# Performance work log

Hardware: AMD Instinct MI355X
Metric: run time of the kernel (lower is better)

The kernel has to match this reference:

```python
import jax, jax.numpy as jnp
import numpy as np
from jax import lax

K = 3
PAD = 1
K2 = K * K


def _conv(x, w, b):
    dn = lax.conv_dimension_numbers(x.shape, w.shape, ('NCHW', 'OIHW', 'NCHW'))
    y = lax.conv_general_dilated(x, w, (1, 1), [(PAD, PAD), (PAD, PAD)], dimension_numbers=dn)
    return y + b[None, :, None, None]


def _gather(x, iy, ix):
    # x: [B,C,H,W]; iy,ix: [B,K2,H,W] int32 -> [B,C,K2,H,W]
    B, C, H, W = x.shape
    flat = x.reshape(B, C, H * W)
    idx = iy * W + ix  # [B,K2,H,W]
    return jax.vmap(lambda xb, ib: xb[:, ib])(flat, idx)


def _deform_conv2d(x, offset_w, offset_b, mask_w, mask_b, weight):
    B, C, H, W = x.shape
    O = weight.shape[0]
    offset = _conv(x, offset_w, offset_b)            # [B,2*K2,H,W]
    mask = jax.nn.sigmoid(_conv(x, mask_w, mask_b))  # [B,K2,H,W]

    off = offset.reshape(B, K2, 2, H, W)
    oy, ox = off[:, :, 0], off[:, :, 1]              # [B,K2,H,W]

    ki = (jnp.arange(K2) // K).astype(x.dtype)       # kernel row per tap
    kj = (jnp.arange(K2) % K).astype(x.dtype)        # kernel col per tap
    base_y = (jnp.arange(H) - PAD).astype(x.dtype)
    base_x = (jnp.arange(W) - PAD).astype(x.dtype)

    py = oy + base_y[None, None, :, None] + ki[None, :, None, None]  # [B,K2,H,W]
    px = ox + base_x[None, None, None, :] + kj[None, :, None, None]

    y0 = jnp.floor(py)
    x0 = jnp.floor(px)
    dy = py - y0
    dx = px - x0
    y0i = y0.astype(jnp.int32)
    x0i = x0.astype(jnp.int32)

    acc = jnp.zeros((B, C, K2, H, W), dtype=x.dtype)
    for (yc, xc, wgt) in [
        (y0i,     x0i,     (1 - dy) * (1 - dx)),
        (y0i,     x0i + 1, (1 - dy) * dx),
        (y0i + 1, x0i,     dy * (1 - dx)),
        (y0i + 1, x0i + 1, dy * dx),
    ]:
        valid = ((yc >= 0) & (yc < H) & (xc >= 0) & (xc < W)).astype(x.dtype)
        g = _gather(x, jnp.clip(yc, 0, H - 1), jnp.clip(xc, 0, W - 1))  # [B,C,K2,H,W]
        acc = acc + g * (wgt * valid)[:, None]

    modulated = acc * mask[:, None]                  # [B,C,K2,H,W]
    w2 = weight.reshape(O, C, K2)
    return jnp.einsum('bckhw,ock->bohw', modulated, w2)


def setup_inputs() -> dict:
    key = jax.random.key(0)
    ks = jax.random.split(key, 6)
    B, C, O, H, W = 4, 64, 64, 128, 128
    return {
        'x': jax.random.normal(ks[0], (B, C, H, W), jnp.float32),
        'offset_w': jax.random.normal(ks[1], (2 * K2, C, K, K), jnp.float32) * 0.05,
        'offset_b': jax.random.normal(ks[2], (2 * K2,), jnp.float32) * 0.05,
        'mask_w': jax.random.normal(ks[3], (K2, C, K, K), jnp.float32) * 0.05,
        'mask_b': jnp.full((K2,), 0.5, jnp.float32),
        'weight': jax.random.normal(ks[5], (O, C, K, K), jnp.float32) * (1.0 / np.sqrt(C * K2)),
    }


def reference(x, offset_w, offset_b, mask_w, mask_b, weight):
    return _deform_conv2d(x, offset_w, offset_b, mask_w, mask_b, weight)
```

## Files before the change

kernel.cpp:

```cpp
#include <hip/hip_runtime.h>
#include <math.h>

#define BB 4
#define CC 64
#define OO 64
#define HH 128
#define WW 128
#define HWsz (HH * WW)

typedef __attribute__((ext_vector_type(8))) _Float16 half8;
typedef __attribute__((ext_vector_type(4))) float floatx4;

__global__ __launch_bounds__(256) void pre_kernel(
    const float* __restrict__ x, const float* __restrict__ wgt,
    const float* __restrict__ ow, const float* __restrict__ mw,
    _Float16* __restrict__ xh, _Float16* __restrict__ waf,
    _Float16* __restrict__ wcf)
{
    int bid = blockIdx.x;
    int tid = threadIdx.x;
    if (bid < 512) {
        int b = bid >> 7, y = bid & 127;
        int px = tid & 127;
        int ch = (tid >> 7) * 32;
        const float* xp = x + (size_t)(b * CC + ch) * HWsz + y * WW + px;
        _Float16 buf[32];
#pragma unroll
        for (int q = 0; q < 32; ++q)
            buf[q] = (_Float16)xp[(size_t)q * HWsz];
        _Float16* dst = xh + ((size_t)(b * HH + y) * WW + px) * 64 + ch;
#pragma unroll
        for (int q = 0; q < 4; ++q)
            *(half8*)&dst[q * 8] = *(const half8*)&buf[q * 8];
    } else {
        int i = (bid - 512) * 256 + tid;
        if (i < 36864) {
            int j = i & 7, lane = (i >> 3) & 63, rest = i >> 9;
            int m = rest & 3, kh = (rest >> 2) & 1, k = rest >> 3;
            int o = m * 16 + (lane & 15);
            int c = kh * 32 + ((lane >> 4) << 3) + j;
            waf[i] = (_Float16)wgt[o * 576 + c * 9 + k];
        } else if (i < 55296) {
            int t = i - 36864;
            int j = t & 7, lane = (t >> 3) & 63, rest = t >> 9;
            int m = rest & 1, kh = (rest >> 1) & 1, k = rest >> 2;
            int o = m * 16 + (lane & 15);
            int c = kh * 32 + ((lane >> 4) << 3) + j;
            float v = 0.f;
            if (o < 18) v = ow[o * 576 + c * 9 + k];
            else if (o < 27) v = mw[(o - 18) * 576 + c * 9 + k];
            wcf[t] = (_Float16)v;
        }
    }
}

__global__ __launch_bounds__(1024, 1) void fused_kernel(
    const _Float16* __restrict__ xh, const _Float16* __restrict__ waf,
    const _Float16* __restrict__ wcf, const float* __restrict__ ob,
    const float* __restrict__ mb, float* __restrict__ out)
{
    __shared__ __align__(16) _Float16 lds_waf[36864];
    __shared__ _Float16 omh[16 * 27 * 16];
    __shared__ __align__(16) _Float16 blendb[16 * 2048];

    int tid = threadIdx.x;
    int gid = blockIdx.x;
    int sid = (gid & 7) * 32 + (gid >> 3);
    int b = sid >> 6;
    int t = sid & 63;
    int rq = t >> 1;
    int q = t & 1;

    int wv = tid >> 6;
    int lane = tid & 63;
    int s = wv & 3;
    int h = rq * 4 + (wv >> 2);
    int p0 = q << 6;
    int g = lane >> 4;
    int pl = lane & 15;
    int goff = g * 8;
    int xw = p0 + s * 16 + pl;
    int oct = lane & 7;
    int pxg = lane >> 3;

    const _Float16* xhb = xh + ((size_t)b << 20);
    _Float16* omw = &omh[wv * 27 * 16];
    _Float16* bbw = &blendb[wv * 2048];

    half8 stg[9];
    if (wv < 8) {
#pragma unroll
        for (int i = 0; i < 9; ++i)
            stg[i] = *(const half8*)(waf + ((wv * 9 + i) << 9) + lane * 8);
    }

    floatx4 accC0 = {0.f, 0.f, 0.f, 0.f};
    floatx4 accC1 = {0.f, 0.f, 0.f, 0.f};

#define CADDR(K, P, V) do {                                                  \
    int ky = (K) / 3, kx = (K) - ky * 3;                                     \
    int yy = h + ky - 1, xx = xw + kx - 1;                                   \
    V = (yy >= 0) & (yy < HH) & (xx >= 0) & (xx < WW);                       \
    int yc = min(max(yy, 0), HH - 1), xc = min(max(xx, 0), WW - 1);          \
    P = ((yc * WW + xc) << 6) + goff;                                        \
} while (0)

#define CONVTAP(K, S0, S1, V) do {                                           \
    const _Float16* wp = wcf + ((K) << 11) + lane * 8;                       \
    half8 w00 = *(const half8*)(wp + (0 << 9));                              \
    half8 w01 = *(const half8*)(wp + (1 << 9));                              \
    half8 w10 = *(const half8*)(wp + (2 << 9));                              \
    half8 w11 = *(const half8*)(wp + (3 << 9));                              \
    half8 z = {0, 0, 0, 0, 0, 0, 0, 0};                                     \
    half8 a0 = (V) ? S0 : z;                                                 \
    half8 a1 = (V) ? S1 : z;                                                 \
    accC0 = __builtin_amdgcn_mfma_f32_16x16x32_f16(w00, a0, accC0, 0, 0, 0); \
    accC1 = __builtin_amdgcn_mfma_f32_16x16x32_f16(w01, a0, accC1, 0, 0, 0); \
    accC0 = __builtin_amdgcn_mfma_f32_16x16x32_f16(w10, a1, accC0, 0, 0, 0); \
    accC1 = __builtin_amdgcn_mfma_f32_16x16x32_f16(w11, a1, accC1, 0, 0, 0); \
} while (0)

    {
        bool vA, vB;
        int pa, pb;
        half8 A0, A1, B0, B1;
        CADDR(0, pa, vA);
        A0 = *(const half8*)(xhb + pa);
        A1 = *(const half8*)(xhb + pa + 32);
#pragma unroll 1
        for (int kp = 0; kp < 4; ++kp) {
            int k = kp * 2;
            CADDR(k + 1, pb, vB);
            B0 = *(const half8*)(xhb + pb);
            B1 = *(const half8*)(xhb + pb + 32);
            CONVTAP(k, A0, A1, vA);
            CADDR(k + 2, pa, vA);
            A0 = *(const half8*)(xhb + pa);
            A1 = *(const half8*)(xhb + pa + 32);
            CONVTAP(k + 1, B0, B1, vB);
        }
        CONVTAP(8, A0, A1, vA);
    }

#pragma unroll
    for (int j = 0; j < 4; ++j) {
        int o = g * 4 + j;
        omw[o * 16 + pl] = (_Float16)(accC0[j] + ob[o]);
        int o2 = 16 + g * 4 + j;
        float v = accC1[j];
        if (o2 < 18) omw[o2 * 16 + pl] = (_Float16)(v + ob[o2]);
        else if (o2 < 27)
            omw[o2 * 16 + pl] =
                (_Float16)(1.0f / (1.0f + expf(-(v + mb[o2 - 18]))));
    }

    if (wv < 8) {
#pragma unroll
        for (int i = 0; i < 9; ++i)
            *(half8*)&lds_waf[((wv * 9 + i) << 9) + lane * 8] = stg[i];
    }
    __syncthreads();

    floatx4 acc0 = {0.f, 0.f, 0.f, 0.f}, acc1 = {0.f, 0.f, 0.f, 0.f};
    floatx4 acc2 = {0.f, 0.f, 0.f, 0.f}, acc3 = {0.f, 0.f, 0.f, 0.f};

#define MKT(K, P, U00, U01, U10, U11, I00, I01, I10, I11) do {               \
    int ky = (K) / 3, kx = (K) - ky * 3;                                     \
    float oy = (float)omw[(2 * (K)) * 16 + (P)];                             \
    float ox = (float)omw[(2 * (K) + 1) * 16 + (P)];                         \
    float mk = (float)omw[(18 + (K)) * 16 + (P)];                            \
    float py = oy + (float)(h + ky - 1);                                     \
    float qx = ox + (float)(p0 + s * 16 + (P) + kx - 1);                     \
    float y0f = floorf(py), x0f = floorf(qx);                                \
    float dyy = py - y0f, dxx = qx - x0f;                                    \
    int y0 = (int)y0f, x0 = (int)x0f;                                        \
    int y1 = y0 + 1, x1 = x0 + 1;                                            \
    bool vy0 = (y0 >= 0) & (y0 < HH), vy1 = (y1 >= 0) & (y1 < HH);           \
    bool vx0 = (x0 >= 0) & (x0 < WW), vx1 = (x1 >= 0) & (x1 < WW);           \
    U00 = (vy0 & vx0) ? (1.f - dyy) * (1.f - dxx) * mk : 0.f;                \
    U01 = (vy0 & vx1) ? (1.f - dyy) * dxx * mk : 0.f;                        \
    U10 = (vy1 & vx0) ? dyy * (1.f - dxx) * mk : 0.f;                        \
    U11 = (vy1 & vx1) ? dyy * dxx * mk : 0.f;                                \
    int yc0 = min(max(y0, 0), HH - 1), yc1 = min(max(y1, 0), HH - 1);        \
    int xc0 = min(max(x0, 0), WW - 1), xc1 = min(max(x1, 0), WW - 1);        \
    I00 = ((yc0 * WW + xc0) << 6) + oct * 8;                                 \
    I01 = ((yc0 * WW + xc1) << 6) + oct * 8;                                 \
    I10 = ((yc1 * WW + xc0) << 6) + oct * 8;                                 \
    I11 = ((yc1 * WW + xc1) << 6) + oct * 8;                                 \
} while (0)

#define SPLAT8(H) ((half8){(H), (H), (H), (H), (H), (H), (H), (H)})
#define MF(Q, B, A) A = __builtin_amdgcn_mfma_f32_16x16x32_f16(Q, B, A, 0, 0, 0)

#define TAP(K) do {                                                          \
    float uA0, uA1, uA2, uA3, uB0, uB1, uB2, uB3;                            \
    int iA0, iA1, iA2, iA3, iB0, iB1, iB2, iB3;                              \
    MKT(K, pxg, uA0, uA1, uA2, uA3, iA0, iA1, iA2, iA3);                     \
    MKT(K, 8 + pxg, uB0, uB1, uB2, uB3, iB0, iB1, iB2, iB3);                 \
    half8 a0 = *(const half8*)(xhb + iA0);                                   \
    half8 a1 = *(const half8*)(xhb + iA1);                                   \
    half8 a2 = *(const half8*)(xhb + iA2);                                   \
    half8 a3 = *(const half8*)(xhb + iA3);                                   \
    half8 e0 = *(const half8*)(xhb + iB0);                                   \
    half8 e1 = *(const half8*)(xhb + iB1);                                   \
    half8 e2 = *(const half8*)(xhb + iB2);                                   \
    half8 e3 = *(const half8*)(xhb + iB3);                                   \
    half8 bfA = a0 * SPLAT8((_Float16)uA0);                                  \
    bfA = bfA + a1 * SPLAT8((_Float16)uA1);                                  \
    bfA = bfA + a2 * SPLAT8((_Float16)uA2);                                  \
    bfA = bfA + a3 * SPLAT8((_Float16)uA3);                                  \
    half8 bfB = e0 * SPLAT8((_Float16)uB0);                                  \
    bfB = bfB + e1 * SPLAT8((_Float16)uB1);                                  \
    bfB = bfB + e2 * SPLAT8((_Float16)uB2);                                  \
    bfB = bfB + e3 * SPLAT8((_Float16)uB3);                                  \
    _Float16* bb = bbw + (((K) & 1) << 10);                                  \
    *(half8*)&bb[(pxg << 6) + ((oct ^ pxg) << 3)] = bfA;                     \
    *(half8*)&bb[((8 + pxg) << 6) + ((oct ^ pxg) << 3)] = bfB;               \
    half8 bf = *(const half8*)&bb[(pl << 6) + ((g ^ (pl & 7)) << 3)];        \
    half8 bd = *(const half8*)&bb[(pl << 6) + (((g + 4) ^ (pl & 7)) << 3)];  \
    const _Float16* wk = &lds_waf[((K) << 12) + lane * 8];                   \
    half8 q0 = *(const half8*)(wk + (0 << 9));                               \
    half8 q1 = *(const half8*)(wk + (1 << 9));                               \
    half8 q2 = *(const half8*)(wk + (2 << 9));                               \
    half8 q3 = *(const half8*)(wk + (3 << 9));                               \
    half8 q4 = *(const half8*)(wk + (4 << 9));                               \
    half8 q5 = *(const half8*)(wk + (5 << 9));                               \
    half8 q6 = *(const half8*)(wk + (6 << 9));                               \
    half8 q7 = *(const half8*)(wk + (7 << 9));                               \
    MF(q0, bf, acc0); MF(q1, bf, acc1); MF(q2, bf, acc2); MF(q3, bf, acc3);  \
    MF(q4, bd, acc0); MF(q5, bd, acc1); MF(q6, bd, acc2); MF(q7, bd, acc3);  \
} while (0)

    TAP(0); TAP(1); TAP(2); TAP(3); TAP(4); TAP(5); TAP(6); TAP(7); TAP(8);

    float* outp = out + (size_t)b * OO * HWsz + h * WW + p0 + s * 16 + pl;
#pragma unroll
    for (int j = 0; j < 4; ++j) outp[(size_t)(g * 4 + j) * HWsz] = acc0[j];
#pragma unroll
    for (int j = 0; j < 4; ++j) outp[(size_t)(16 + g * 4 + j) * HWsz] = acc1[j];
#pragma unroll
    for (int j = 0; j < 4; ++j) outp[(size_t)(32 + g * 4 + j) * HWsz] = acc2[j];
#pragma unroll
    for (int j = 0; j < 4; ++j) outp[(size_t)(48 + g * 4 + j) * HWsz] = acc3[j];
}

extern "C" void kernel_launch(void* const* d_in, const int* in_sizes, int n_in,
                              void* d_out, int out_size, void* d_ws, size_t ws_size,
                              hipStream_t stream)
{
    const float* x   = (const float*)d_in[0];
    const float* ow  = (const float*)d_in[1];
    const float* ob  = (const float*)d_in[2];
    const float* mw  = (const float*)d_in[3];
    const float* mb  = (const float*)d_in[4];
    const float* wgt = (const float*)d_in[5];
    float* out = (float*)d_out;

    _Float16* xh  = (_Float16*)d_ws;
    _Float16* waf = xh + (size_t)BB * HWsz * 64;
    _Float16* wcf = waf + 36864;

    pre_kernel<<<dim3(512 + 216), dim3(256), 0, stream>>>(
        x, wgt, ow, mw, xh, waf, wcf);
    fused_kernel<<<dim3(256), dim3(1024), 0, stream>>>(
        xh, waf, wcf, ob, mb, out);
}
```

Before: 44.30 us.

## Stage conv input rows in LDS and preload all weights into shared memory

The offset/mask conv now loads each input row segment (18 pixels × 64 channels) into a per-wave LDS bounce buffer once and reuses it across the three horizontal taps, instead of issuing separate global loads per tap. Both the main weights and the offset/mask conv weights are copied cooperatively into LDS at kernel start, replacing the register-staged copy that only covered the main weights. The blend buffer is shrunk from a double buffer to a single one that is shared with the conv staging. The intent is fewer global loads for the conv. The cost is a full barrier before any compute starts and removal of the double buffering in the blend stage, which could add LDS hazards or stalls between taps.

Result: faster. 37.43 us (-15.5%).

```diff
diff --git a/kernel.cpp b/kernel.cpp
--- a/kernel.cpp
+++ b/kernel.cpp
@@ -55,13 +55,13 @@
 }
 
 __global__ __launch_bounds__(1024, 1) void fused_kernel(
-    const _Float16* __restrict__ xh, const _Float16* __restrict__ waf,
-    const _Float16* __restrict__ wcf, const float* __restrict__ ob,
-    const float* __restrict__ mb, float* __restrict__ out)
+    const _Float16* __restrict__ wsrc, const _Float16* __restrict__ xh,
+    const float* __restrict__ ob, const float* __restrict__ mb,
+    float* __restrict__ out)
 {
-    __shared__ __align__(16) _Float16 lds_waf[36864];
+    __shared__ __align__(16) _Float16 lds_w[55296];
     __shared__ _Float16 omh[16 * 27 * 16];
-    __shared__ __align__(16) _Float16 blendb[16 * 2048];
+    __shared__ __align__(16) _Float16 bounce[16 * 1152];
 
     int tid = threadIdx.x;
     int gid = blockIdx.x;
@@ -78,69 +78,59 @@
     int p0 = q << 6;
     int g = lane >> 4;
     int pl = lane & 15;
-    int goff = g * 8;
-    int xw = p0 + s * 16 + pl;
     int oct = lane & 7;
     int pxg = lane >> 3;
 
     const _Float16* xhb = xh + ((size_t)b << 20);
     _Float16* omw = &omh[wv * 27 * 16];
-    _Float16* bbw = &blendb[wv * 2048];
-
-    half8 stg[9];
-    if (wv < 8) {
-#pragma unroll
-        for (int i = 0; i < 9; ++i)
-            stg[i] = *(const half8*)(waf + ((wv * 9 + i) << 9) + lane * 8);
+    _Float16* bbw = &bounce[wv * 1152];
+
+#pragma unroll
+    for (int it = 0; it < 7; ++it) {
+        int c = it * 1024 + tid;
+        if (c < 6912)
+            *(half8*)&lds_w[c * 8] = *(const half8*)(wsrc + c * 8);
     }
+    __syncthreads();
 
     floatx4 accC0 = {0.f, 0.f, 0.f, 0.f};
     floatx4 accC1 = {0.f, 0.f, 0.f, 0.f};
 
-#define CADDR(K, P, V) do {                                                  \
-    int ky = (K) / 3, kx = (K) - ky * 3;                                     \
-    int yy = h + ky - 1, xx = xw + kx - 1;                                   \
-    V = (yy >= 0) & (yy < HH) & (xx >= 0) & (xx < WW);                       \
-    int yc = min(max(yy, 0), HH - 1), xc = min(max(xx, 0), WW - 1);          \
-    P = ((yc * WW + xc) << 6) + goff;                                        \
-} while (0)
-
-#define CONVTAP(K, S0, S1, V) do {                                           \
-    const _Float16* wp = wcf + ((K) << 11) + lane * 8;                       \
+#define STAGE_ROW(KY) do {                                                   \
+    int gy = h + (KY) - 1;                                                   \
+    half8 z = {0, 0, 0, 0, 0, 0, 0, 0};                                      \
+    _Pragma("unroll") for (int j = 0; j < 3; ++j) {                          \
+        int pxi = j * 8 + pxg;                                               \
+        bool act = (j < 2) | (pxg < 2);                                      \
+        int col = p0 + s * 16 - 1 + pxi;                                     \
+        bool val = act & (gy >= 0) & (gy < HH) & (col >= 0) & (col < WW);    \
+        half8 v = z;                                                         \
+        if (val)                                                             \
+            v = *(const half8*)(xhb + (((size_t)gy * WW + col) << 6) + oct * 8); \
+        if (act)                                                             \
+            *(half8*)&bbw[(pxi << 6) + ((oct ^ (pxi & 7)) << 3)] = v;        \
+    }                                                                        \
+} while (0)
+
+#define CONVT(KY, KX) do {                                                   \
+    int K = (KY) * 3 + (KX);                                                 \
+    int pc = pl + (KX);                                                      \
+    half8 a0 = *(const half8*)&bbw[(pc << 6) + ((g ^ (pc & 7)) << 3)];       \
+    half8 a1 = *(const half8*)&bbw[(pc << 6) + (((g + 4) ^ (pc & 7)) << 3)]; \
+    const _Float16* wp = &lds_w[36864 + (K << 11) + lane * 8];               \
     half8 w00 = *(const half8*)(wp + (0 << 9));                              \
     half8 w01 = *(const half8*)(wp + (1 << 9));                              \
     half8 w10 = *(const half8*)(wp + (2 << 9));                              \
     half8 w11 = *(const half8*)(wp + (3 << 9));                              \
-    half8 z = {0, 0, 0, 0, 0, 0, 0, 0};                                     \
-    half8 a0 = (V) ? S0 : z;                                                 \
-    half8 a1 = (V) ? S1 : z;                                                 \
     accC0 = __builtin_amdgcn_mfma_f32_16x16x32_f16(w00, a0, accC0, 0, 0, 0); \
     accC1 = __builtin_amdgcn_mfma_f32_16x16x32_f16(w01, a0, accC1, 0, 0, 0); \
     accC0 = __builtin_amdgcn_mfma_f32_16x16x32_f16(w10, a1, accC0, 0, 0, 0); \
     accC1 = __builtin_amdgcn_mfma_f32_16x16x32_f16(w11, a1, accC1, 0, 0, 0); \
 } while (0)
 
-    {
-        bool vA, vB;
-        int pa, pb;
-        half8 A0, A1, B0, B1;
-        CADDR(0, pa, vA);
-        A0 = *(const half8*)(xhb + pa);
-        A1 = *(const half8*)(xhb + pa + 32);
-#pragma unroll 1
-        for (int kp = 0; kp < 4; ++kp) {
-            int k = kp * 2;
-            CADDR(k + 1, pb, vB);
-            B0 = *(const half8*)(xhb + pb);
-            B1 = *(const half8*)(xhb + pb + 32);
-            CONVTAP(k, A0, A1, vA);
-            CADDR(k + 2, pa, vA);
-            A0 = *(const half8*)(xhb + pa);
-            A1 = *(const half8*)(xhb + pa + 32);
-            CONVTAP(k + 1, B0, B1, vB);
-        }
-        CONVTAP(8, A0, A1, vA);
-    }
+    STAGE_ROW(0); CONVT(0, 0); CONVT(0, 1); CONVT(0, 2);
+    STAGE_ROW(1); CONVT(1, 0); CONVT(1, 1); CONVT(1, 2);
+    STAGE_ROW(2); CONVT(2, 0); CONVT(2, 1); CONVT(2, 2);
 
 #pragma unroll
     for (int j = 0; j < 4; ++j) {
@@ -153,13 +143,6 @@
             omw[o2 * 16 + pl] =
                 (_Float16)(1.0f / (1.0f + expf(-(v + mb[o2 - 18]))));
     }
-
-    if (wv < 8) {
-#pragma unroll
-        for (int i = 0; i < 9; ++i)
-            *(half8*)&lds_waf[((wv * 9 + i) << 9) + lane * 8] = stg[i];
-    }
-    __syncthreads();
 
     floatx4 acc0 = {0.f, 0.f, 0.f, 0.f}, acc1 = {0.f, 0.f, 0.f, 0.f};
     floatx4 acc2 = {0.f, 0.f, 0.f, 0.f}, acc3 = {0.f, 0.f, 0.f, 0.f};
@@ -213,12 +196,11 @@
     bfB = bfB + e1 * SPLAT8((_Float16)uB1);                                  \
     bfB = bfB + e2 * SPLAT8((_Float16)uB2);                                  \
     bfB = bfB + e3 * SPLAT8((_Float16)uB3);                                  \
-    _Float16* bb = bbw + (((K) & 1) << 10);                                  \
-    *(half8*)&bb[(pxg << 6) + ((oct ^ pxg) << 3)] = bfA;                     \
-    *(half8*)&bb[((8 + pxg) << 6) + ((oct ^ pxg) << 3)] = bfB;               \
-    half8 bf = *(const half8*)&bb[(pl << 6) + ((g ^ (pl & 7)) << 3)];        \
-    half8 bd = *(const half8*)&bb[(pl << 6) + (((g + 4) ^ (pl & 7)) << 3)];  \
-    const _Float16* wk = &lds_waf[((K) << 12) + lane * 8];                   \
+    *(half8*)&bbw[(pxg << 6) + ((oct ^ pxg) << 3)] = bfA;                    \
+    *(half8*)&bbw[((8 + pxg) << 6) + ((oct ^ pxg) << 3)] = bfB;              \
+    half8 bf = *(const half8*)&bbw[(pl << 6) + ((g ^ (pl & 7)) << 3)];       \
+    half8 bd = *(const half8*)&bbw[(pl << 6) + (((g + 4) ^ (pl & 7)) << 3)]; \
+    const _Float16* wk = &lds_w[((K) << 12) + lane * 8];                     \
     half8 q0 = *(const half8*)(wk + (0 << 9));                               \
     half8 q1 = *(const half8*)(wk + (1 << 9));                               \
     half8 q2 = *(const half8*)(wk + (2 << 9));                               \
@@ -263,5 +245,5 @@
     pre_kernel<<<dim3(512 + 216), dim3(256), 0, stream>>>(
         x, wgt, ow, mw, xh, waf, wcf);
     fused_kernel<<<dim3(256), dim3(1024), 0, stream>>>(
-        xh, waf, wcf, ob, mb, out);
+        waf, xh, ob, mb, out);
 }
```
